# Kernel optimization log

Measured on AMD Instinct MI355X. Metric: run time of the kernel, lower is better.

## Reference

```python
import jax, jax.numpy as jnp
import numpy as np

EMBED_DIM = 1024
SCALE = float(np.sqrt(EMBED_DIM))


def setup_inputs() -> dict:
    key = jax.random.key(0)
    ks = jax.random.split(key, 4)
    B, S, D = 4, 2048, EMBED_DIM
    x = jax.random.normal(ks[0], (B, S, D), dtype=jnp.float32)
    # causal mask: 1 where attention allowed, 0 where blocked
    mask = jnp.tril(jnp.ones((S, S), dtype=jnp.int32))
    init = 1.0 / np.sqrt(D)
    Wq = jax.random.normal(ks[1], (D, D), dtype=jnp.float32) * init
    Wk = jax.random.normal(ks[2], (D, D), dtype=jnp.float32) * init
    Wv = jax.random.normal(ks[3], (D, D), dtype=jnp.float32) * init
    bq = jnp.zeros((D,), dtype=jnp.float32)
    bk = jnp.zeros((D,), dtype=jnp.float32)
    bv = jnp.zeros((D,), dtype=jnp.float32)
    return {"x": x, "mask": mask, "Wq": Wq, "bq": bq, "Wk": Wk, "bk": bk, "Wv": Wv, "bv": bv}


def reference(x, mask, Wq, bq, Wk, bk, Wv, bv):
    # Q, K, V projections (torch Linear: x @ W^T + b; here W stored as (D_in, D_out))
    q = x @ Wq + bq  # (B, S, D)
    k = x @ Wk + bk
    v = x @ Wv + bv
    # attention scores: Q K^T / sqrt(D)
    scores = jnp.einsum("bsd,btd->bst", q, k) / SCALE  # (B, S, S)
    scores = jnp.where(mask == 0, -jnp.inf, scores)
    attn = jax.nn.softmax(scores, axis=-1)
    # dropout disabled (inference / eval mode)
    out = jnp.einsum("bst,btd->bsd", attn, v)  # (B, S, D)
    return out
```

## Files before the change

kernel.cpp:

```cpp
#include <hip/hip_runtime.h>
#include <math.h>

#define DMODEL 1024
#define SEQ 2048
#define BATCH 4
#define SCALE_INV (1.0f/32.0f)

typedef unsigned short ushort_t;
typedef __attribute__((ext_vector_type(8))) short bf16x8;
typedef __attribute__((ext_vector_type(4))) float f32x4;

__device__ __forceinline__ ushort_t f2bf(float f) {
    unsigned int u = __float_as_uint(f);
    unsigned int rounding = 0x7FFFu + ((u >> 16) & 1u);
    return (ushort_t)((u + rounding) >> 16);
}

#define GLOAD16(SRC, DST) \
    __builtin_amdgcn_global_load_lds( \
        (const __attribute__((address_space(1))) void*)(SRC), \
        (__attribute__((address_space(3))) void*)(DST), 16, 0, 0)

__device__ __forceinline__ int xcd_swz(int bid, int nwg) {
    return (bid & 7) * (nwg >> 3) + (bid >> 3);
}

#define STAGE_TILE(ASP, BSP, K0) do { \
    _Pragma("unroll") \
    for (int i_ = 0; i_ < 2; ++i_) { \
        const int off_ = i_ * 4096 + w * 1024 + l * 16; \
        const int row_ = off_ >> 6; \
        const int ke_  = (off_ & 63) >> 1; \
        GLOAD16(A + (size_t)(arow0 + row_) * lda + (K0) + ke_, \
                (char*)(ASP) + i_ * 4096 + w * 1024); \
    } \
    _Pragma("unroll") \
    for (int i_ = 0; i_ < 2; ++i_) { \
        const int off_ = i_ * 4096 + w * 1024 + l * 16; \
        const int row_ = off_ >> 6; \
        const int ke_  = (off_ & 63) >> 1; \
        GLOAD16(Bt + (size_t)(brow0 + row_) * ldb + (K0) + ke_, \
                (char*)(BSP) + i_ * 4096 + w * 1024); \
    } \
} while (0)

#define COMPUTE_TILE(ASP, BSP) do { \
    bf16x8 a_[4], b_[4]; \
    _Pragma("unroll") \
    for (int m_ = 0; m_ < 4; ++m_) \
        a_[m_] = *(const bf16x8*)((ASP) + (wr * 64 + m_ * 16 + (l & 15)) * 32 + (l >> 4) * 8); \
    _Pragma("unroll") \
    for (int n_ = 0; n_ < 4; ++n_) \
        b_[n_] = *(const bf16x8*)((BSP) + (wc * 64 + n_ * 16 + (l & 15)) * 32 + (l >> 4) * 8); \
    _Pragma("unroll") \
    for (int m_ = 0; m_ < 4; ++m_) \
        _Pragma("unroll") \
        for (int n_ = 0; n_ < 4; ++n_) \
            acc[m_][n_] = __builtin_amdgcn_mfma_f32_16x16x32_bf16(a_[m_], b_[n_], acc[m_][n_], 0, 0, 0); \
} while (0)

__device__ __forceinline__ void gemm_core_128(
    const ushort_t* __restrict__ A, int lda,
    const ushort_t* __restrict__ Bt, int ldb,
    int arow0, int brow0, int ksteps,
    ushort_t* As0, ushort_t* Bs0, ushort_t* As1, ushort_t* Bs1,
    f32x4 acc[4][4])
{
    const int tid = threadIdx.x;
    const int l   = tid & 63;
    const int w   = tid >> 6;
    const int wr  = w >> 1;
    const int wc  = w & 1;

    STAGE_TILE(As0, Bs0, 0);
    __syncthreads();

    int s = 0;
    while (true) {
        if (s + 1 < ksteps) STAGE_TILE(As1, Bs1, (s + 1) * 32);
        COMPUTE_TILE(As0, Bs0);
        __syncthreads();
        if (++s >= ksteps) break;

        if (s + 1 < ksteps) STAGE_TILE(As0, Bs0, (s + 1) * 32);
        COMPUTE_TILE(As1, Bs1);
        __syncthreads();
        if (++s >= ksteps) break;
    }
}

__global__ __launch_bounds__(256) void qkv_gemm_mfma(
    const ushort_t* __restrict__ x,
    const ushort_t* __restrict__ wt,
    const float* __restrict__ bq, const float* __restrict__ bk, const float* __restrict__ bv,
    ushort_t* __restrict__ q, ushort_t* __restrict__ k, ushort_t* __restrict__ vt)
{
    __shared__ __align__(16) ushort_t As0[128 * 32];
    __shared__ __align__(16) ushort_t Bs0[128 * 32];
    __shared__ __align__(16) ushort_t As1[128 * 32];
    __shared__ __align__(16) ushort_t Bs1[128 * 32];

    const int wg = xcd_swz(blockIdx.x, 8 * 64 * 3);
    const int z  = wg >> 9;
    const int r  = wg & 511;
    const int by = r >> 3;
    const int bx = r & 7;

    const ushort_t* Bt = wt + (size_t)z * DMODEL * DMODEL;
    const float* bias = (z == 0) ? bq : (z == 1) ? bk : bv;
    const float scale = (z == 0) ? SCALE_INV : 1.0f;

    const int arow0 = by * 128;
    const int brow0 = bx * 128;

    f32x4 acc[4][4];
    #pragma unroll
    for (int m = 0; m < 4; ++m)
        #pragma unroll
        for (int n = 0; n < 4; ++n)
            acc[m][n] = (f32x4)(0.f);

    gemm_core_128(x, DMODEL, Bt, DMODEL, arow0, brow0, DMODEL / 32,
                  As0, Bs0, As1, Bs1, acc);

    const int l  = threadIdx.x & 63;
    const int w  = threadIdx.x >> 6;
    const int wr = w >> 1, wc = w & 1;

    if (z < 2) {
        ushort_t* out = (z == 0) ? q : k;
        #pragma unroll
        for (int n = 0; n < 4; ++n) {
            const int gcol = brow0 + wc * 64 + n * 16 + (l & 15);
            const float bb = bias[gcol];
            #pragma unroll
            for (int m = 0; m < 4; ++m) {
                #pragma unroll
                for (int j = 0; j < 4; ++j) {
                    const int grow = arow0 + wr * 64 + m * 16 + (l >> 4) * 4 + j;
                    out[(size_t)grow * DMODEL + gcol] = f2bf((acc[m][n][j] + bb) * scale);
                }
            }
        }
    } else {
        ushort_t* vtb = vt + (size_t)(arow0 >> 11) * DMODEL * SEQ;
        #pragma unroll
        for (int n = 0; n < 4; ++n) {
            const int gcol = brow0 + wc * 64 + n * 16 + (l & 15);
            const float bb = bias[gcol];
            #pragma unroll
            for (int m = 0; m < 4; ++m) {
                const int t0 = (arow0 & 2047) + wr * 64 + m * 16 + (l >> 4) * 4;
                ushort4 o;
                o.x = f2bf(acc[m][n][0] + bb);
                o.y = f2bf(acc[m][n][1] + bb);
                o.z = f2bf(acc[m][n][2] + bb);
                o.w = f2bf(acc[m][n][3] + bb);
                *(ushort4*)(vtb + (size_t)gcol * SEQ + t0) = o;
            }
        }
    }
}

__global__ __launch_bounds__(256) void qkt_exp_mfma(
    const ushort_t* __restrict__ q, const ushort_t* __restrict__ k,
    ushort_t* __restrict__ P, float* __restrict__ partials)
{
    const int wg = xcd_swz(blockIdx.x, 544);
    const int b  = wg / 136;
    const int i  = wg - b * 136;
    int st = (int)((sqrtf(8.f * (float)i + 1.f) - 1.f) * 0.5f);
    if (st * (st + 1) / 2 > i) st--;
    else if ((st + 1) * (st + 2) / 2 <= i) st++;
    const int tt = i - st * (st + 1) / 2;

    __shared__ __align__(16) ushort_t As0[128 * 32];
    __shared__ __align__(16) ushort_t Bs0[128 * 32];
    __shared__ __align__(16) ushort_t As1[128 * 32];
    __shared__ __align__(16) ushort_t Bs1[128 * 32];

    const ushort_t* A  = q + (size_t)b * SEQ * DMODEL;
    const ushort_t* Bt = k + (size_t)b * SEQ * DMODEL;

    f32x4 acc[4][4];
    #pragma unroll
    for (int m = 0; m < 4; ++m)
        #pragma unroll
        for (int n = 0; n < 4; ++n)
            acc[m][n] = (f32x4)(0.f);

    gemm_core_128(A, DMODEL, Bt, DMODEL, st * 128, tt * 128, DMODEL / 32,
                  As0, Bs0, As1, Bs1, acc);

    const int l  = threadIdx.x & 63;
    const int w  = threadIdx.x >> 6;
    const int wr = w >> 1, wc = w & 1;
    ushort_t* pb = P + (size_t)b * SEQ * SEQ;
    float* part = partials + ((size_t)b * 32 + (size_t)(tt * 2 + wc)) * SEQ;
    const bool diag = (st == tt);

    #pragma unroll
    for (int m = 0; m < 4; ++m) {
        #pragma unroll
        for (int j = 0; j < 4; ++j) {
            const int grow = st * 128 + wr * 64 + m * 16 + (l >> 4) * 4 + j;
            float rs = 0.f;
            #pragma unroll
            for (int n = 0; n < 4; ++n) {
                const int gcol = tt * 128 + wc * 64 + n * 16 + (l & 15);
                float e = 0.f;
                if (!diag || gcol <= grow) e = __expf(acc[m][n][j]);
                rs += e;
                pb[(size_t)grow * SEQ + gcol] = f2bf(e);
            }
            rs += __shfl_xor(rs, 1);
            rs += __shfl_xor(rs, 2);
            rs += __shfl_xor(rs, 4);
            rs += __shfl_xor(rs, 8);
            if ((l & 15) == 0) part[grow] = rs;
        }
    }
}

__global__ __launch_bounds__(256) void pv_gemm_mfma(
    const ushort_t* __restrict__ P, const ushort_t* __restrict__ vt,
    const float* __restrict__ partials, float* __restrict__ outp)
{
    const int wg = xcd_swz(blockIdx.x, 8 * 16 * BATCH);
    const int b  = wg >> 7;
    const int r  = wg & 127;
    const int st = r >> 3;
    const int dt = r & 7;

    __shared__ __align__(16) ushort_t As0[128 * 32];
    __shared__ __align__(16) ushort_t Bs0[128 * 32];
    __shared__ __align__(16) ushort_t As1[128 * 32];
    __shared__ __align__(16) ushort_t Bs1[128 * 32];
    __shared__ float inv_lds[128];

    const int tid = threadIdx.x;
    if (tid < 128) {
        const int grow = st * 128 + tid;
        const int hmax = (st + 1) * 2;
        float ssum = 0.f;
        for (int h = 0; h < hmax; ++h)
            ssum += partials[((size_t)b * 32 + h) * SEQ + grow];
        inv_lds[tid] = 1.0f / ssum;
    }

    const ushort_t* A  = P + (size_t)b * SEQ * SEQ;
    const ushort_t* Bt = vt + (size_t)b * DMODEL * SEQ;
    float* out = outp + (size_t)b * SEQ * DMODEL;

    f32x4 acc[4][4];
    #pragma unroll
    for (int m = 0; m < 4; ++m)
        #pragma unroll
        for (int n = 0; n < 4; ++n)
            acc[m][n] = (f32x4)(0.f);

    const int ksteps = (st + 1) * 4;
    gemm_core_128(A, SEQ, Bt, SEQ, st * 128, dt * 128, ksteps,
                  As0, Bs0, As1, Bs1, acc);

    const int l  = threadIdx.x & 63;
    const int w  = threadIdx.x >> 6;
    const int wr = w >> 1, wc = w & 1;
    #pragma unroll
    for (int m = 0; m < 4; ++m) {
        #pragma unroll
        for (int j = 0; j < 4; ++j) {
            const int lrow = wr * 64 + m * 16 + (l >> 4) * 4 + j;
            const int grow = st * 128 + lrow;
            const float iv = inv_lds[lrow];
            #pragma unroll
            for (int n = 0; n < 4; ++n) {
                const int gcol = dt * 128 + wc * 64 + n * 16 + (l & 15);
                out[(size_t)grow * DMODEL + gcol] = acc[m][n][j] * iv;
            }
        }
    }
}

__global__ __launch_bounds__(256) void prep_kernel(
    const float* __restrict__ x, ushort_t* __restrict__ x_bf,
    const float* __restrict__ Wq, const float* __restrict__ Wk, const float* __restrict__ Wv,
    ushort_t* __restrict__ wt)
{
    __shared__ float tile[32][33];
    const int bid = blockIdx.x;
    const int tid = threadIdx.x;

    if (bid < 8192) {
        const int i = bid * 256 + tid;
        const float4 f = *(const float4*)(x + (size_t)i * 4);
        ushort4 o;
        o.x = f2bf(f.x); o.y = f2bf(f.y); o.z = f2bf(f.z); o.w = f2bf(f.w);
        *(ushort4*)(x_bf + (size_t)i * 4) = o;
    } else {
        const int id = bid - 8192;
        const int z  = id >> 10;
        const int t  = id & 1023;
        const int k0 = (t & 31) * 32;
        const int n0 = (t >> 5) * 32;
        const float* W = (z == 0) ? Wq : (z == 1) ? Wk : Wv;
        ushort_t* wtd = wt + (size_t)z * DMODEL * DMODEL;
        const int x_ = tid & 31, y = tid >> 5;
        #pragma unroll
        for (int i = 0; i < 4; ++i)
            tile[y + i * 8][x_] = W[(size_t)(k0 + y + i * 8) * DMODEL + n0 + x_];
        __syncthreads();
        #pragma unroll
        for (int i = 0; i < 4; ++i)
            wtd[(size_t)(n0 + y + i * 8) * DMODEL + k0 + x_] = f2bf(tile[x_][y + i * 8]);
    }
}

__global__ __launch_bounds__(1024) void qkv_gemm_f32(
    const float* __restrict__ x,
    const float* __restrict__ Wq, const float* __restrict__ bq,
    const float* __restrict__ Wk, const float* __restrict__ bk,
    const float* __restrict__ Wv, const float* __restrict__ bv,
    float* __restrict__ q, float* __restrict__ k, float* __restrict__ v)
{
    const float* W; const float* bias; float* out;
    const int z = blockIdx.z;
    if (z == 0)      { W = Wq; bias = bq; out = q; }
    else if (z == 1) { W = Wk; bias = bk; out = k; }
    else             { W = Wv; bias = bv; out = v; }

    __shared__ float As[32][33];
    __shared__ float Bs[32][33];
    const int tx = threadIdx.x, ty = threadIdx.y;
    const int row = blockIdx.y * 32 + ty;
    const int col = blockIdx.x * 32 + tx;

    float acc = 0.f;
    for (int k0 = 0; k0 < DMODEL; k0 += 32) {
        As[ty][tx] = x[(size_t)row * DMODEL + k0 + tx];
        Bs[ty][tx] = W[(size_t)(k0 + ty) * DMODEL + col];
        __syncthreads();
        #pragma unroll
        for (int kk = 0; kk < 32; ++kk)
            acc += As[ty][kk] * Bs[kk][tx];
        __syncthreads();
    }
    out[(size_t)row * DMODEL + col] = acc + bias[col];
}

__global__ __launch_bounds__(256) void attn_f32(
    const float* __restrict__ q, const float* __restrict__ k,
    const float* __restrict__ v, float* __restrict__ out)
{
    const int s = blockIdx.x, b = blockIdx.y, tid = threadIdx.x;
    __shared__ float qs[DMODEL];
    __shared__ float sc[SEQ];
    __shared__ float red[256];
    const float* qrow = q + ((size_t)b * SEQ + s) * DMODEL;
    for (int d = tid; d < DMODEL; d += 256) qs[d] = qrow[d];
    __syncthreads();
    const float* kb = k + (size_t)b * SEQ * DMODEL;
    const int nt = s + 1;
    float lmax = -INFINITY;
    for (int t = tid; t < nt; t += 256) {
        const float* krow = kb + (size_t)t * DMODEL;
        float acc = 0.f;
        for (int d = 0; d < DMODEL; d += 4) {
            const float4 kv = *(const float4*)(krow + d);
            acc += qs[d] * kv.x + qs[d+1] * kv.y + qs[d+2] * kv.z + qs[d+3] * kv.w;
        }
        acc *= SCALE_INV; sc[t] = acc; lmax = fmaxf(lmax, acc);
    }
    red[tid] = lmax; __syncthreads();
    for (int off = 128; off > 0; off >>= 1) { if (tid < off) red[tid] = fmaxf(red[tid], red[tid+off]); __syncthreads(); }
    const float mx = red[0]; __syncthreads();
    float lsum = 0.f;
    for (int t = tid; t < nt; t += 256) { const float e = expf(sc[t]-mx); sc[t]=e; lsum+=e; }
    red[tid] = lsum; __syncthreads();
    for (int off = 128; off > 0; off >>= 1) { if (tid < off) red[tid] += red[tid+off]; __syncthreads(); }
    const float inv = 1.0f / red[0]; __syncthreads();
    const float* vb = v + (size_t)b * SEQ * DMODEL;
    float a0=0,a1=0,a2=0,a3=0;
    for (int t = 0; t < nt; ++t) {
        const float p = sc[t];
        const float* vrow = vb + (size_t)t * DMODEL;
        a0 += p*vrow[tid]; a1 += p*vrow[tid+256]; a2 += p*vrow[tid+512]; a3 += p*vrow[tid+768];
    }
    float* orow = out + ((size_t)b * SEQ + s) * DMODEL;
    orow[tid]=a0*inv; orow[tid+256]=a1*inv; orow[tid+512]=a2*inv; orow[tid+768]=a3*inv;
}

extern "C" void kernel_launch(void* const* d_in, const int* in_sizes, int n_in,
                              void* d_out, int out_size, void* d_ws, size_t ws_size,
                              hipStream_t stream)
{
    const float* x  = (const float*)d_in[0];
    const float* Wq = (const float*)d_in[2];
    const float* bq = (const float*)d_in[3];
    const float* Wk = (const float*)d_in[4];
    const float* bk = (const float*)d_in[5];
    const float* Wv = (const float*)d_in[6];
    const float* bv = (const float*)d_in[7];
    float* out = (float*)d_out;

    const size_t SZ_XBF  = (size_t)BATCH * SEQ * DMODEL * 2;
    const size_t SZ_WT   = 3 * (size_t)DMODEL * DMODEL * 2;
    const size_t SZ_QKV  = (size_t)BATCH * SEQ * DMODEL * 2;
    const size_t SZ_P    = (size_t)BATCH * SEQ * SEQ * 2;
    const size_t SZ_PART = (size_t)BATCH * 32 * SEQ * 4;
    const size_t NEED = SZ_XBF + SZ_WT + 3 * SZ_QKV + SZ_P + SZ_PART;

    if (ws_size >= NEED) {
        char* p = (char*)d_ws;
        ushort_t* x_bf = (ushort_t*)p;              p += SZ_XBF;
        ushort_t* wt   = (ushort_t*)p;              p += SZ_WT;
        ushort_t* q_bf = (ushort_t*)p;              p += SZ_QKV;
        ushort_t* k_bf = (ushort_t*)p;              p += SZ_QKV;
        ushort_t* vt   = (ushort_t*)p;              p += SZ_QKV;
        ushort_t* Pb   = (ushort_t*)p;              p += SZ_P;
        float*    part = (float*)p;

        hipLaunchKernelGGL(prep_kernel, dim3(8192 + 3072), dim3(256), 0, stream,
                           x, x_bf, Wq, Wk, Wv, wt);
        hipLaunchKernelGGL(qkv_gemm_mfma, dim3(8 * 64 * 3), dim3(256), 0, stream,
                           x_bf, wt, bq, bk, bv, q_bf, k_bf, vt);
        hipLaunchKernelGGL(qkt_exp_mfma, dim3(544), dim3(256), 0, stream,
                           q_bf, k_bf, Pb, part);
        hipLaunchKernelGGL(pv_gemm_mfma, dim3(8 * 16 * BATCH), dim3(256), 0, stream,
                           Pb, vt, part, out);
    } else {
        const size_t elems = (size_t)BATCH * SEQ * DMODEL;
        float* q = (float*)d_ws;
        float* k = q + elems;
        float* v = k + elems;
        hipLaunchKernelGGL(qkv_gemm_f32, dim3(DMODEL / 32, BATCH * SEQ / 32, 3), dim3(32, 32), 0, stream,
                           x, Wq, bq, Wk, bk, Wv, bv, q, k, v);
        hipLaunchKernelGGL(attn_f32, dim3(SEQ, BATCH), dim3(256), 0, stream, q, k, v, out);
    }
}
```

Measured before the change: 171.4 us.

## Triple-buffer LDS tiles with explicit vmcnt waits in shared GEMM core

```diff
diff --git a/kernel.cpp b/kernel.cpp
--- a/kernel.cpp
+++ b/kernel.cpp
@@ -59,11 +59,20 @@
             acc[m_][n_] = __builtin_amdgcn_mfma_f32_16x16x32_bf16(a_[m_], b_[n_], acc[m_][n_], 0, 0, 0); \
 } while (0)
 
+#define VM_WAIT4() asm volatile("s_waitcnt vmcnt(4)" ::: "memory")
+#define VM_WAIT0() asm volatile("s_waitcnt vmcnt(0)" ::: "memory")
+#define END_BARRIER() do { \
+    asm volatile("s_waitcnt lgkmcnt(0)" ::: "memory"); \
+    __builtin_amdgcn_s_barrier(); \
+    asm volatile("" ::: "memory"); \
+} while (0)
+
 __device__ __forceinline__ void gemm_core_128(
     const ushort_t* __restrict__ A, int lda,
     const ushort_t* __restrict__ Bt, int ldb,
     int arow0, int brow0, int ksteps,
     ushort_t* As0, ushort_t* Bs0, ushort_t* As1, ushort_t* Bs1,
+    ushort_t* As2, ushort_t* Bs2,
     f32x4 acc[4][4])
 {
     const int tid = threadIdx.x;
@@ -73,18 +82,29 @@
     const int wc  = w & 1;
 
     STAGE_TILE(As0, Bs0, 0);
-    __syncthreads();
+    STAGE_TILE(As1, Bs1, 32);
+    VM_WAIT4();
+    __builtin_amdgcn_s_barrier();
+    asm volatile("" ::: "memory");
 
     int s = 0;
     while (true) {
-        if (s + 1 < ksteps) STAGE_TILE(As1, Bs1, (s + 1) * 32);
+        if (s + 2 < ksteps) { STAGE_TILE(As2, Bs2, (s + 2) * 32); VM_WAIT4(); }
+        else if (s + 1 < ksteps) { VM_WAIT0(); }
         COMPUTE_TILE(As0, Bs0);
-        __syncthreads();
+        END_BARRIER();
         if (++s >= ksteps) break;
 
-        if (s + 1 < ksteps) STAGE_TILE(As0, Bs0, (s + 1) * 32);
+        if (s + 2 < ksteps) { STAGE_TILE(As0, Bs0, (s + 2) * 32); VM_WAIT4(); }
+        else if (s + 1 < ksteps) { VM_WAIT0(); }
         COMPUTE_TILE(As1, Bs1);
-        __syncthreads();
+        END_BARRIER();
+        if (++s >= ksteps) break;
+
+        if (s + 2 < ksteps) { STAGE_TILE(As1, Bs1, (s + 2) * 32); VM_WAIT4(); }
+        else if (s + 1 < ksteps) { VM_WAIT0(); }
+        COMPUTE_TILE(As2, Bs2);
+        END_BARRIER();
         if (++s >= ksteps) break;
     }
 }
@@ -99,6 +119,8 @@
     __shared__ __align__(16) ushort_t Bs0[128 * 32];
     __shared__ __align__(16) ushort_t As1[128 * 32];
     __shared__ __align__(16) ushort_t Bs1[128 * 32];
+    __shared__ __align__(16) ushort_t As2[128 * 32];
+    __shared__ __align__(16) ushort_t Bs2[128 * 32];
 
     const int wg = xcd_swz(blockIdx.x, 8 * 64 * 3);
     const int z  = wg >> 9;
@@ -121,7 +143,7 @@
             acc[m][n] = (f32x4)(0.f);
 
     gemm_core_128(x, DMODEL, Bt, DMODEL, arow0, brow0, DMODEL / 32,
-                  As0, Bs0, As1, Bs1, acc);
+                  As0, Bs0, As1, Bs1, As2, Bs2, acc);
 
     const int l  = threadIdx.x & 63;
     const int w  = threadIdx.x >> 6;
@@ -178,6 +200,8 @@
     __shared__ __align__(16) ushort_t Bs0[128 * 32];
     __shared__ __align__(16) ushort_t As1[128 * 32];
     __shared__ __align__(16) ushort_t Bs1[128 * 32];
+    __shared__ __align__(16) ushort_t As2[128 * 32];
+    __shared__ __align__(16) ushort_t Bs2[128 * 32];
 
     const ushort_t* A  = q + (size_t)b * SEQ * DMODEL;
     const ushort_t* Bt = k + (size_t)b * SEQ * DMODEL;
@@ -190,7 +214,7 @@
             acc[m][n] = (f32x4)(0.f);
 
     gemm_core_128(A, DMODEL, Bt, DMODEL, st * 128, tt * 128, DMODEL / 32,
-                  As0, Bs0, As1, Bs1, acc);
+                  As0, Bs0, As1, Bs1, As2, Bs2, acc);
 
     const int l  = threadIdx.x & 63;
     const int w  = threadIdx.x >> 6;
@@ -236,6 +260,8 @@
     __shared__ __align__(16) ushort_t Bs0[128 * 32];
     __shared__ __align__(16) ushort_t As1[128 * 32];
     __shared__ __align__(16) ushort_t Bs1[128 * 32];
+    __shared__ __align__(16) ushort_t As2[128 * 32];
+    __shared__ __align__(16) ushort_t Bs2[128 * 32];
     __shared__ float inv_lds[128];
 
     const int tid = threadIdx.x;
@@ -261,7 +287,7 @@
 
     const int ksteps = (st + 1) * 4;
     gemm_core_128(A, SEQ, Bt, SEQ, st * 128, dt * 128, ksteps,
-                  As0, Bs0, As1, Bs1, acc);
+                  As0, Bs0, As1, Bs1, As2, Bs2, acc);
 
     const int l  = threadIdx.x & 63;
     const int w  = threadIdx.x >> 6;
```

After: 181.6 us. 6.0% more time.
